# Kernel tuning notes

Measured on AMD Instinct MI355X. Metric: run time of the kernel, lower is better.

Reference implementation:

```python
import jax, jax.numpy as jnp
import numpy as np

N = 10000          # nodes
E_RAND = 320000    # random edges (avg degree 32)
F_IN = 512         # nfeat
HID = 256          # args.hid
HEADS = 8          # args.head
FH = HID // HEADS  # 32 per head
NCLASS = 40
TAU = 0.5
LAMDA = 0.5
K = 2


def setup_inputs() -> dict:
    key = jax.random.key(0)
    ks = jax.random.split(key, 16)
    # edge list: random edges + self-loops (so every dst segment is non-empty)
    src = jnp.concatenate([jax.random.randint(ks[0], (E_RAND,), 0, N), jnp.arange(N)])
    dst = jnp.concatenate([jax.random.randint(ks[1], (E_RAND,), 0, N), jnp.arange(N)])
    s = 0.05  # small init scale keeps exp() in attention/bind_loss stable
    return {
        "x": jax.random.normal(ks[2], (N, F_IN), jnp.float32),
        "src": src, "dst": dst,
        "W0": jax.random.normal(ks[3], (F_IN, HEADS, FH), jnp.float32) * s,
        "a0s": jax.random.normal(ks[4], (HEADS, FH), jnp.float32) * s,
        "a0d": jax.random.normal(ks[5], (HEADS, FH), jnp.float32) * s,
        "W1": jax.random.normal(ks[6], (HID, HEADS, FH), jnp.float32) * s,
        "a1s": jax.random.normal(ks[7], (HEADS, FH), jnp.float32) * s,
        "a1d": jax.random.normal(ks[8], (HEADS, FH), jnp.float32) * s,
        "W2": jax.random.normal(ks[9], (HID, HEADS, FH), jnp.float32) * s,
        "a2s": jax.random.normal(ks[10], (HEADS, FH), jnp.float32) * s,
        "a2d": jax.random.normal(ks[11], (HEADS, FH), jnp.float32) * s,
        "Wout": jax.random.normal(ks[12], (HID, HEADS, NCLASS), jnp.float32) * s,
        "aos": jax.random.normal(ks[13], (HEADS, NCLASS), jnp.float32) * s,
        "aod": jax.random.normal(ks[14], (HEADS, NCLASS), jnp.float32) * s,
    }


def _gat_layer(x, W, a_s, a_d, src, dst):
    """Sparse multi-head GAT layer: gather -> edge softmax -> scatter."""
    n = x.shape[0]
    h = jnp.einsum('nf,fhd->nhd', x, W)              # [N,H,Fh]
    es = jnp.sum(h * a_s, axis=-1)                    # [N,H]
    ed = jnp.sum(h * a_d, axis=-1)                    # [N,H]
    e = jax.nn.leaky_relu(es[src] + ed[dst], 0.2)     # [E,H]
    m = jax.ops.segment_max(e, dst, num_segments=n)   # per-dst max (stable softmax)
    w = jnp.exp(e - m[dst])
    z = jax.ops.segment_sum(w, dst, num_segments=n)
    alpha = w / z[dst]                                # [E,H]
    return jax.ops.segment_sum(alpha[:, :, None] * h[src], dst, num_segments=n)  # [N,H,Fh]


def _bind_loss(z):
    # z1 == z2 == z in the original call site: refl_sim == between_sim
    zn = z / jnp.maximum(jnp.linalg.norm(z, axis=1, keepdims=True), 1e-12)
    S = jnp.exp(jnp.matmul(zn, zn.T) / TAU)           # [N,N]
    d = jnp.diagonal(S)
    off = jnp.sum(S, axis=1) - d                      # masked (off-diagonal) row sum
    CT = -jnp.log(d / (off + off))                    # neg_c2.sum + neg_c3.sum
    return jnp.mean(CT)


def reference(x, src, dst, W0, a0s, a0d, W1, a1s, a1d, W2, a2s, a2d, Wout, aos, aod):
    layers = [(W0, a0s, a0d), (W1, a1s, a1d), (W2, a2s, a2d)]
    last = x
    loss = jnp.float32(0.0)
    for i, (W, as_, ad_) in enumerate(layers):
        cur = jax.nn.elu(_gat_layer(last, W, as_, ad_, src, dst))
        cur = cur.reshape(cur.shape[0], -1)           # concat heads -> [N, HID]
        if i > 0:
            beta = LAMDA / (i + 2)                    # MaskLayer(last, cur, lamda, i+2)
            cur = beta * last + (1.0 - beta) * cur
            if i % K == 0:
                loss = loss + _bind_loss(cur)
        last = cur
    out = _gat_layer(last, Wout, aos, aod, src, dst).mean(axis=1)  # avg heads -> [N,C]
    return (jax.nn.log_softmax(out, axis=1), loss)
```

## Files before the change

### kernel.cpp

```cpp
#include <hip/hip_runtime.h>
#include <hip/hip_bf16.h>
#include <math.h>

#define NN_F_IN   512
#define NN_HID    256
#define NN_HEADS  8
#define NN_FH     32
#define NN_NCLASS 40
#define TAU_F     0.5f
#define LAMDA_F   0.5f
#define ZN_SCALE  1.6986436f

typedef __attribute__((ext_vector_type(8))) short bf16x8;
typedef __attribute__((ext_vector_type(4))) float f32x4;

static __device__ __forceinline__ float lrelu02(float x) { return x >= 0.f ? x : 0.2f * x; }
static __device__ __forceinline__ float elu1(float x)    { return x > 0.f ? x : expm1f(x); }
static __device__ __forceinline__ float b2f(unsigned short u) {
    unsigned int x = ((unsigned int)u) << 16;
    return __uint_as_float(x);
}
static __device__ __forceinline__ unsigned short f2b(float f) {
    __hip_bfloat16 hb = __float2bfloat16(f);
    return *reinterpret_cast<unsigned short*>(&hb);
}

__global__ void prep_count_kernel(const float* __restrict__ x,
                                  const float* __restrict__ W0, const float* __restrict__ W1,
                                  const float* __restrict__ W2, const float* __restrict__ Wo,
                                  unsigned short* __restrict__ Xb,
                                  unsigned short* __restrict__ Wt0, unsigned short* __restrict__ Wt1,
                                  unsigned short* __restrict__ Wt2, unsigned short* __restrict__ Wto,
                                  int n4X,
                                  const int* __restrict__ dst, int* __restrict__ counts,
                                  int E, int nCountB) {
    if (blockIdx.x < nCountB) {
        int e = blockIdx.x * 256 + threadIdx.x;
        if (e < E) atomicAdd(&counts[dst[e]], 1);
        return;
    }
    int i = (blockIdx.x - nCountB) * 256 + threadIdx.x;
    if (i < n4X) {
        float4 v = *(const float4*)(x + (size_t)i * 4);
        ushort4 o;
        o.x = f2b(v.x); o.y = f2b(v.y); o.z = f2b(v.z); o.w = f2b(v.w);
        *(ushort4*)(Xb + (size_t)i * 4) = o;
        return;
    }
    i -= n4X;
    if (i < 256 * 512) {
        int np = i >> 9, k = i & 511;
        Wt0[i] = f2b(W0[(size_t)k * 256 + np]);
        return;
    }
    i -= 256 * 512;
    if (i < 256 * 256) {
        int np = i >> 8, k = i & 255;
        Wt1[i] = f2b(W1[(size_t)k * 256 + np]);
        return;
    }
    i -= 256 * 256;
    if (i < 256 * 256) {
        int np = i >> 8, k = i & 255;
        Wt2[i] = f2b(W2[(size_t)k * 256 + np]);
        return;
    }
    i -= 256 * 256;
    if (i < 384 * 256) {
        int np = i >> 8, k = i & 255;
        Wto[i] = f2b(np < 320 ? Wo[(size_t)k * 320 + np] : 0.f);
    }
}

__global__ __launch_bounds__(256) void fc_attn_mfma(
    const unsigned short* __restrict__ A, const unsigned short* __restrict__ B,
    unsigned short* __restrict__ H, const float* __restrict__ As_,
    const float* __restrict__ Ad_, float* __restrict__ es, float* __restrict__ ed,
    int M, int K) {
    const int ldH = 256;
    int t = threadIdx.x, lane = t & 63, wid = t >> 6;
    int wrow = wid >> 1, wcol = wid & 1;
    int l15 = lane & 15, lg = lane >> 4;
    int mbase = blockIdx.y * 64 + wrow * 32;
    int nbase = blockIdx.x * 64 + wcol * 32;

    const unsigned short* Ap[2];
    const unsigned short* Bp[2];
#pragma unroll
    for (int m = 0; m < 2; ++m) {
        int rr = mbase + m * 16 + l15;
        if (rr > M - 1) rr = M - 1;
        Ap[m] = A + (size_t)rr * K + lg * 8;
        Bp[m] = B + (size_t)(nbase + m * 16 + l15) * K + lg * 8;
    }
    f32x4 acc[2][2];
#pragma unroll
    for (int m = 0; m < 2; ++m)
#pragma unroll
        for (int nn = 0; nn < 2; ++nn)
#pragma unroll
            for (int r = 0; r < 4; ++r) acc[m][nn][r] = 0.f;

    bf16x8 aP[2], bP[2], aQ[2], bQ[2];
#pragma unroll
    for (int m = 0; m < 2; ++m) {
        aP[m] = *(const bf16x8*)(Ap[m]);
        bP[m] = *(const bf16x8*)(Bp[m]);
    }
    int nhalf = K >> 6;
    int kk = 32;
    for (int it = 0; it < nhalf; ++it) {
#pragma unroll
        for (int m = 0; m < 2; ++m) {
            aQ[m] = *(const bf16x8*)(Ap[m] + kk);
            bQ[m] = *(const bf16x8*)(Bp[m] + kk);
        }
#pragma unroll
        for (int m = 0; m < 2; ++m)
#pragma unroll
            for (int nn = 0; nn < 2; ++nn)
                acc[m][nn] = __builtin_amdgcn_mfma_f32_16x16x32_bf16(aP[m], bP[nn], acc[m][nn], 0, 0, 0);
        if (it + 1 < nhalf) {
#pragma unroll
            for (int m = 0; m < 2; ++m) {
                aP[m] = *(const bf16x8*)(Ap[m] + kk + 32);
                bP[m] = *(const bf16x8*)(Bp[m] + kk + 32);
            }
        }
#pragma unroll
        for (int m = 0; m < 2; ++m)
#pragma unroll
            for (int nn = 0; nn < 2; ++nn)
                acc[m][nn] = __builtin_amdgcn_mfma_f32_16x16x32_bf16(aQ[m], bQ[nn], acc[m][nn], 0, 0, 0);
        kk += 64;
    }
#pragma unroll
    for (int m = 0; m < 2; ++m) {
#pragma unroll
        for (int nn = 0; nn < 2; ++nn) {
            int col = nbase + nn * 16 + l15;
#pragma unroll
            for (int r = 0; r < 4; ++r) {
                int row = mbase + m * 16 + lg * 4 + r;
                if (row < M) H[(size_t)row * ldH + col] = f2b(acc[m][nn][r]);
            }
        }
    }
    int hh = blockIdx.x * 2 + wcol;
    float a0 = As_[hh * 32 + l15], a1 = As_[hh * 32 + 16 + l15];
    float d0 = Ad_[hh * 32 + l15], d1 = Ad_[hh * 32 + 16 + l15];
#pragma unroll
    for (int m = 0; m < 2; ++m) {
#pragma unroll
        for (int r = 0; r < 4; ++r) {
            float ps = acc[m][0][r] * a0 + acc[m][1][r] * a1;
            float pd = acc[m][0][r] * d0 + acc[m][1][r] * d1;
            ps += __shfl_xor(ps, 1, 64); pd += __shfl_xor(pd, 1, 64);
            ps += __shfl_xor(ps, 2, 64); pd += __shfl_xor(pd, 2, 64);
            ps += __shfl_xor(ps, 4, 64); pd += __shfl_xor(pd, 4, 64);
            ps += __shfl_xor(ps, 8, 64); pd += __shfl_xor(pd, 8, 64);
            if (l15 == 0) {
                int row = mbase + m * 16 + lg * 4 + r;
                if (row < M) {
                    es[row * NN_HEADS + hh] = ps;
                    ed[row * NN_HEADS + hh] = pd;
                }
            }
        }
    }
}

__global__ void scan_kernel(const int* __restrict__ counts, int* __restrict__ row_start,
                            int* __restrict__ cursor, int n) {
    __shared__ int s[1024];
    int t  = threadIdx.x;
    int ch = (n + 1023) / 1024;
    int lo = t * ch;
    int sum = 0;
    for (int j = 0; j < ch; ++j) {
        int i = lo + j;
        if (i < n) sum += counts[i];
    }
    s[t] = sum;
    __syncthreads();
    for (int off = 1; off < 1024; off <<= 1) {
        int v = 0;
        if (t >= off) v = s[t - off];
        __syncthreads();
        s[t] += v;
        __syncthreads();
    }
    int run = (t == 0) ? 0 : s[t - 1];
    for (int j = 0; j < ch; ++j) {
        int i = lo + j;
        if (i < n) {
            row_start[i] = run;
            cursor[i] = run;
            run += counts[i];
        }
    }
    if (t == 1023) row_start[n] = s[1023];
}

__global__ void scatter_kernel(const int* __restrict__ src, const int* __restrict__ dst,
                               int* __restrict__ cursor, int* __restrict__ csr_src, int E) {
    int e = blockIdx.x * blockDim.x + threadIdx.x;
    if (e < E) {
        int d   = dst[e];
        int pos = atomicAdd(&cursor[d], 1);
        csr_src[pos] = src[e];
    }
}

__global__ __launch_bounds__(256) void gather_hidden(
    const unsigned short* __restrict__ Hm, const float* __restrict__ es,
    const float* __restrict__ ed, const int* __restrict__ csr_src,
    const int* __restrict__ row_start, const unsigned short* __restrict__ last,
    unsigned short* __restrict__ out, int n, float beta,
    unsigned short* __restrict__ znb, float* __restrict__ dvec) {
    int lane = threadIdx.x & 63;
    int nn   = blockIdx.x * 4 + (threadIdx.x >> 6);
    if (nn >= n) return;
    int s0 = row_start[nn], s1 = row_start[nn + 1];
    int h2 = lane >> 3;
    float edh = ed[nn * NN_HEADS + h2];

    float zacc = 0.f;
    float a0 = 0.f, a1 = 0.f, a2 = 0.f, a3 = 0.f;
    int fullEnd = s0 + ((s1 - s0) & ~7);
    int e = s0;
    for (; e < fullEnd; e += 8) {
        int idx[8];
        float q[8];
#pragma unroll
        for (int j = 0; j < 8; ++j) idx[j] = csr_src[e + j];
#pragma unroll
        for (int j = 0; j < 8; ++j) q[j] = es[idx[j] * NN_HEADS + h2];
        ushort4 r[8];
#pragma unroll
        for (int j = 0; j < 8; ++j) r[j] = *(const ushort4*)&Hm[(size_t)idx[j] * NN_HID + lane * 4];
#pragma unroll
        for (int j = 0; j < 8; ++j) {
            float w = __expf(lrelu02(q[j] + edh));
            zacc += w;
            a0 += w * b2f(r[j].x); a1 += w * b2f(r[j].y);
            a2 += w * b2f(r[j].z); a3 += w * b2f(r[j].w);
        }
    }
    if (e < s1) {
        int c = s1 - e;
        int idx[8];
        float q[8];
#pragma unroll
        for (int j = 0; j < 8; ++j) idx[j] = csr_src[(j < c) ? e + j : e];
#pragma unroll
        for (int j = 0; j < 8; ++j) q[j] = es[idx[j] * NN_HEADS + h2];
        ushort4 r[8];
#pragma unroll
        for (int j = 0; j < 8; ++j) r[j] = *(const ushort4*)&Hm[(size_t)idx[j] * NN_HID + lane * 4];
#pragma unroll
        for (int j = 0; j < 8; ++j) {
            if (j < c) {
                float w = __expf(lrelu02(q[j] + edh));
                zacc += w;
                a0 += w * b2f(r[j].x); a1 += w * b2f(r[j].y);
                a2 += w * b2f(r[j].z); a3 += w * b2f(r[j].w);
            }
        }
    }
    float zi = 1.f / zacc;
    float v0 = elu1(a0 * zi), v1 = elu1(a1 * zi), v2 = elu1(a2 * zi), v3 = elu1(a3 * zi);
    if (beta >= 0.f) {
        ushort4 lv = *(const ushort4*)&last[(size_t)nn * NN_HID + lane * 4];
        v0 = beta * b2f(lv.x) + (1.f - beta) * v0;
        v1 = beta * b2f(lv.y) + (1.f - beta) * v1;
        v2 = beta * b2f(lv.z) + (1.f - beta) * v2;
        v3 = beta * b2f(lv.w) + (1.f - beta) * v3;
    }
    ushort4 o;
    o.x = f2b(v0); o.y = f2b(v1); o.z = f2b(v2); o.w = f2b(v3);
    *(ushort4*)&out[(size_t)nn * NN_HID + lane * 4] = o;

    if (znb) {
        float ss = v0 * v0 + v1 * v1 + v2 * v2 + v3 * v3;
        ss += __shfl_xor(ss, 1, 64);
        ss += __shfl_xor(ss, 2, 64);
        ss += __shfl_xor(ss, 4, 64);
        ss += __shfl_xor(ss, 8, 64);
        ss += __shfl_xor(ss, 16, 64);
        ss += __shfl_xor(ss, 32, 64);
        float m = fmaxf(sqrtf(ss), 1e-12f);
        float sc = ZN_SCALE / m;
        ushort4 zo;
        zo.x = f2b(v0 * sc); zo.y = f2b(v1 * sc);
        zo.z = f2b(v2 * sc); zo.w = f2b(v3 * sc);
        *(ushort4*)&znb[(size_t)nn * NN_HID + lane * 4] = zo;
        if (lane == 0) dvec[nn] = __expf((ss / (m * m)) * (1.f / TAU_F));
    }
}

__global__ __launch_bounds__(256) void gram_fc_mfma(
    const short* __restrict__ znb, float* __restrict__ P2d, int n,
    int T, int nwg, int Npad,
    const unsigned short* __restrict__ A, const unsigned short* __restrict__ Bw,
    unsigned short* __restrict__ H, int M, int nfc, int fcX) {
    __shared__ short As[2][128 * 64];
    __shared__ short Bs[2][128 * 64];

    int t    = threadIdx.x;
    int lane = t & 63;
    int wid  = t >> 6;
    int l15  = lane & 15, lg = lane >> 4;

    if (blockIdx.x < nfc) {
        const int K = 256, ncols = 320, ldH = 320;
        int idx = blockIdx.x;
        int bx = idx % fcX, by = idx / fcX;
        int wrow = wid >> 1, wcol = wid & 1;
        int mbase = by * 64 + wrow * 32;
        int nbase = bx * 64 + wcol * 32;

        const unsigned short* Ap[2];
        const unsigned short* Bp[2];
#pragma unroll
        for (int m = 0; m < 2; ++m) {
            int rr = mbase + m * 16 + l15;
            if (rr > M - 1) rr = M - 1;
            Ap[m] = A + (size_t)rr * K + lg * 8;
            Bp[m] = Bw + (size_t)(nbase + m * 16 + l15) * K + lg * 8;
        }
        f32x4 acc[2][2];
#pragma unroll
        for (int m = 0; m < 2; ++m)
#pragma unroll
            for (int nn = 0; nn < 2; ++nn)
#pragma unroll
                for (int r = 0; r < 4; ++r) acc[m][nn][r] = 0.f;

        bf16x8 aP[2], bP[2], aQ[2], bQ[2];
#pragma unroll
        for (int m = 0; m < 2; ++m) {
            aP[m] = *(const bf16x8*)(Ap[m]);
            bP[m] = *(const bf16x8*)(Bp[m]);
        }
        int kk = 32;
#pragma unroll
        for (int it = 0; it < 4; ++it) {
#pragma unroll
            for (int m = 0; m < 2; ++m) {
                aQ[m] = *(const bf16x8*)(Ap[m] + kk);
                bQ[m] = *(const bf16x8*)(Bp[m] + kk);
            }
#pragma unroll
            for (int m = 0; m < 2; ++m)
#pragma unroll
                for (int nn = 0; nn < 2; ++nn)
                    acc[m][nn] = __builtin_amdgcn_mfma_f32_16x16x32_bf16(aP[m], bP[nn], acc[m][nn], 0, 0, 0);
            if (it < 3) {
#pragma unroll
                for (int m = 0; m < 2; ++m) {
                    aP[m] = *(const bf16x8*)(Ap[m] + kk + 32);
                    bP[m] = *(const bf16x8*)(Bp[m] + kk + 32);
                }
            }
#pragma unroll
            for (int m = 0; m < 2; ++m)
#pragma unroll
                for (int nn = 0; nn < 2; ++nn)
                    acc[m][nn] = __builtin_amdgcn_mfma_f32_16x16x32_bf16(aQ[m], bQ[nn], acc[m][nn], 0, 0, 0);
            kk += 64;
        }
#pragma unroll
        for (int m = 0; m < 2; ++m) {
#pragma unroll
            for (int nn = 0; nn < 2; ++nn) {
                int col = nbase + nn * 16 + l15;
                if (col >= ncols) continue;
#pragma unroll
                for (int r = 0; r < 4; ++r) {
                    int row = mbase + m * 16 + lg * 4 + r;
                    if (row < M) H[(size_t)row * ldH + col] = f2b(acc[m][nn][r]);
                }
            }
        }
        return;
    }

    int b = blockIdx.x - nfc;
    int q = nwg >> 3, r8 = nwg & 7, xc = b & 7, oo = b >> 3;
    int sid = (xc < r8 ? xc * (q + 1) : r8 * (q + 1) + (xc - r8) * q) + oo;
    int bi = 0, rem = sid;
    while (rem >= T - bi) { rem -= T - bi; ++bi; }
    int bj = bi + rem;
    int i0 = bi * 128, j0 = bj * 128;

    int wrow = wid >> 1, wcol = wid & 1;
    int srow = lane >> 3;
    int sch  = lane & 7;

    f32x4 acc[4][4];
#pragma unroll
    for (int m = 0; m < 4; ++m)
#pragma unroll
        for (int nn = 0; nn < 4; ++nn)
#pragma unroll
            for (int r = 0; r < 4; ++r) acc[m][nn][r] = 0.f;

    bf16x8 sa[2][4], sb[2][4];
#pragma unroll
    for (int sl = 0; sl < 2; ++sl)
#pragma unroll
        for (int s = 0; s < 4; ++s) {
            int row = wid * 32 + s * 8 + srow;
            int gch = sch ^ (row & 7);
            sa[sl][s] = *(const bf16x8*)(znb + (size_t)(i0 + row) * NN_HID + sl * 64 + gch * 8);
            sb[sl][s] = *(const bf16x8*)(znb + (size_t)(j0 + row) * NN_HID + sl * 64 + gch * 8);
        }

#pragma unroll
    for (int kt = 0; kt < 2; ++kt) {
#pragma unroll
        for (int sl = 0; sl < 2; ++sl)
#pragma unroll
            for (int s = 0; s < 4; ++s) {
                int row = wid * 32 + s * 8 + srow;
                *(bf16x8*)(&As[sl][row * 64 + sch * 8]) = sa[sl][s];
                *(bf16x8*)(&Bs[sl][row * 64 + sch * 8]) = sb[sl][s];
            }
        __syncthreads();
        if (kt == 0) {
#pragma unroll
            for (int sl = 0; sl < 2; ++sl)
#pragma unroll
                for (int s = 0; s < 4; ++s) {
                    int row = wid * 32 + s * 8 + srow;
                    int gch = sch ^ (row & 7);
                    sa[sl][s] = *(const bf16x8*)(znb + (size_t)(i0 + row) * NN_HID + 128 + sl * 64 + gch * 8);
                    sb[sl][s] = *(const bf16x8*)(znb + (size_t)(j0 + row) * NN_HID + 128 + sl * 64 + gch * 8);
                }
        }
#pragma unroll
        for (int sl = 0; sl < 2; ++sl) {
#pragma unroll
            for (int ks = 0; ks < 2; ++ks) {
                bf16x8 av[4], bv[4];
#pragma unroll
                for (int m = 0; m < 4; ++m) {
                    int Ra = wrow * 64 + m * 16 + l15;
                    int Rb = wcol * 64 + m * 16 + l15;
                    int ca = (ks * 4 + lg) ^ (Ra & 7);
                    int cb = (ks * 4 + lg) ^ (Rb & 7);
                    av[m] = *(const bf16x8*)(&As[sl][Ra * 64 + ca * 8]);
                    bv[m] = *(const bf16x8*)(&Bs[sl][Rb * 64 + cb * 8]);
                }
#pragma unroll
                for (int m = 0; m < 4; ++m)
#pragma unroll
                    for (int nn = 0; nn < 4; ++nn)
                        acc[m][nn] = __builtin_amdgcn_mfma_f32_16x16x32_bf16(av[m], bv[nn], acc[m][nn], 0, 0, 0);
            }
        }
        if (kt == 0) __syncthreads();
    }

    int i0w = i0 + wrow * 64;
    int j0w = j0 + wcol * 64;
    bool diag = (bj == bi);
    if (bj == T - 1) {
#pragma unroll
        for (int m = 0; m < 4; ++m)
#pragma unroll
            for (int nn = 0; nn < 4; ++nn) {
                int gj = j0w + nn * 16 + l15;
                bool jok = gj < n;
#pragma unroll
                for (int r = 0; r < 4; ++r) {
                    int gi = i0w + m * 16 + lg * 4 + r;
                    acc[m][nn][r] = (jok && gi < n) ? __builtin_exp2f(acc[m][nn][r]) : 0.f;
                }
            }
    } else {
#pragma unroll
        for (int m = 0; m < 4; ++m)
#pragma unroll
            for (int nn = 0; nn < 4; ++nn)
#pragma unroll
                for (int r = 0; r < 4; ++r)
                    acc[m][nn][r] = __builtin_exp2f(acc[m][nn][r]);
    }
    float* rowslot = P2d + (size_t)(2 * bj + wcol) * Npad;
#pragma unroll
    for (int m = 0; m < 4; ++m) {
#pragma unroll
        for (int r = 0; r < 4; ++r) {
            float v = acc[m][0][r] + acc[m][1][r] + acc[m][2][r] + acc[m][3][r];
            v += __shfl_xor(v, 1, 64);
            v += __shfl_xor(v, 2, 64);
            v += __shfl_xor(v, 4, 64);
            v += __shfl_xor(v, 8, 64);
            if (l15 == 0) {
                int gi = i0w + m * 16 + lg * 4 + r;
                if (gi < n) rowslot[gi] = v;
            }
        }
    }
    if (!diag) {
        float* colslot = P2d + (size_t)(2 * bi + wrow) * Npad;
#pragma unroll
        for (int nn = 0; nn < 4; ++nn) {
            float v = 0.f;
#pragma unroll
            for (int m = 0; m < 4; ++m)
#pragma unroll
                for (int r = 0; r < 4; ++r) v += acc[m][nn][r];
            v += __shfl_xor(v, 16, 64);
            v += __shfl_xor(v, 32, 64);
            if (lg == 0) {
                int gj = j0w + nn * 16 + l15;
                if (gj < n) colslot[gj] = v;
            }
        }
    }
}

__global__ __launch_bounds__(256) void attn_fold_kernel(
    const unsigned short* __restrict__ Hm, const float* __restrict__ As,
    const float* __restrict__ Ad, float* __restrict__ es, float* __restrict__ ed,
    int n, int df, int nAt,
    const float* __restrict__ P2d, float* __restrict__ R, int slots, int Npad) {
    if (blockIdx.x < nAt) {
        int idx = blockIdx.x * 256 + threadIdx.x;
        if (idx >= n * NN_HEADS) return;
        int nn = idx / NN_HEADS, hh = idx - nn * NN_HEADS;
        const unsigned short* hp = Hm + (size_t)nn * NN_HEADS * df + hh * df;
        const float* ap = As + hh * df;
        const float* bp = Ad + hh * df;
        float s1 = 0.f, s2 = 0.f;
        for (int d = 0; d < df; d += 4) {
            ushort4 hv = *(const ushort4*)(hp + d);
            float4 av = *(const float4*)(ap + d);
            float4 bv = *(const float4*)(bp + d);
            float h0 = b2f(hv.x), h1 = b2f(hv.y), h2 = b2f(hv.z), h3 = b2f(hv.w);
            s1 += h0 * av.x + h1 * av.y + h2 * av.z + h3 * av.w;
            s2 += h0 * bv.x + h1 * bv.y + h2 * bv.z + h3 * bv.w;
        }
        es[idx] = s1;
        ed[idx] = s2;
        return;
    }
    int i = (blockIdx.x - nAt) * 256 + threadIdx.x;
    if (i >= n) return;
    const float* p = P2d + i;
    float s0 = 0.f, s1 = 0.f, s2 = 0.f, s3 = 0.f;
    int sl = 0;
    for (; sl + 4 <= slots; sl += 4) {
        s0 += p[(size_t)(sl + 0) * Npad];
        s1 += p[(size_t)(sl + 1) * Npad];
        s2 += p[(size_t)(sl + 2) * Npad];
        s3 += p[(size_t)(sl + 3) * Npad];
    }
    for (; sl < slots; ++sl) s0 += p[(size_t)sl * Npad];
    R[i] = (s0 + s1) + (s2 + s3);
}

__global__ __launch_bounds__(256) void edge_loss_kernel(
    const float* __restrict__ es, const float* __restrict__ ed,
    const int* __restrict__ csr_src, const int* __restrict__ row_start,
    float* __restrict__ wC, float* __restrict__ zinv, int n, int nEw,
    const float* __restrict__ R, const float* __restrict__ dvec,
    float* __restrict__ out_loss) {
    if (blockIdx.x < nEw) {
        int lane = threadIdx.x & 63;
        int nn   = blockIdx.x * 4 + (threadIdx.x >> 6);
        if (nn >= n) return;
        int s0 = row_start[nn], s1 = row_start[nn + 1];
        int h    = lane & 7;
        int slot = lane >> 3;
        float edh = ed[nn * NN_HEADS + h];
        float z = 0.f;
        for (int e = s0 + slot; e < s1; e += 8) {
            int sv = csr_src[e];
            float w = __expf(lrelu02(es[sv * NN_HEADS + h] + edh));
            wC[(size_t)e * NN_HEADS + h] = w;
            z += w;
        }
        z += __shfl_xor(z, 8, 64);
        z += __shfl_xor(z, 16, 64);
        z += __shfl_xor(z, 32, 64);
        if (slot == 0) zinv[nn * NN_HEADS + h] = 1.f / z;
        return;
    }
    __shared__ float s[256];
    int t = threadIdx.x;
    float sum = 0.f;
    for (int i = t; i < n; i += 256) {
        float d   = dvec[i];
        float off = R[i] - d;
        sum += -logf(d / (off + off));
    }
    s[t] = sum;
    __syncthreads();
    for (int o = 128; o > 0; o >>= 1) {
        if (t < o) s[t] += s[t + o];
        __syncthreads();
    }
    if (t == 0) *out_loss = s[0] / n;
}

__global__ void gather_final(const unsigned short* __restrict__ Hm, const float* __restrict__ wC,
                             const float* __restrict__ zinv, const int* __restrict__ csr_src,
                             const int* __restrict__ row_start, float* __restrict__ dout, int n) {
    int nn = blockIdx.x;
    __shared__ float accs[NN_HEADS * NN_NCLASS];
    int t = threadIdx.x;
    int s0 = row_start[nn], s1 = row_start[nn + 1];
    int hh = t / NN_NCLASS;
    float acc = 0.f;
    const int LD = NN_HEADS * NN_NCLASS;
    int fullEnd = s0 + ((s1 - s0) & ~7);
    int e = s0;
    for (; e < fullEnd; e += 8) {
        int idx[8];
        float wv[8];
#pragma unroll
        for (int j = 0; j < 8; ++j) {
            idx[j] = csr_src[e + j];
            wv[j]  = wC[(size_t)(e + j) * NN_HEADS + hh];
        }
        float v[8];
#pragma unroll
        for (int j = 0; j < 8; ++j) v[j] = b2f(Hm[(size_t)idx[j] * LD + t]);
#pragma unroll
        for (int j = 0; j < 8; ++j) acc += wv[j] * v[j];
    }
    if (e < s1) {
        int c = s1 - e;
        int idx[8];
        float wv[8];
#pragma unroll
        for (int j = 0; j < 8; ++j) {
            int p = (j < c) ? e + j : e;
            idx[j] = csr_src[p];
            wv[j]  = wC[(size_t)p * NN_HEADS + hh];
        }
        float v[8];
#pragma unroll
        for (int j = 0; j < 8; ++j) v[j] = b2f(Hm[(size_t)idx[j] * LD + t]);
#pragma unroll
        for (int j = 0; j < 8; ++j) {
            if (j < c) acc += wv[j] * v[j];
        }
    }
    accs[t] = acc * zinv[nn * NN_HEADS + hh];
    __syncthreads();
    if (t < 64) {
        float v = -INFINITY;
        if (t < NN_NCLASS) {
            float sacc = 0.f;
#pragma unroll
            for (int h2 = 0; h2 < NN_HEADS; ++h2) sacc += accs[h2 * NN_NCLASS + t];
            v = sacc * (1.f / NN_HEADS);
        }
        float mx = v;
#pragma unroll
        for (int o = 1; o < 64; o <<= 1) mx = fmaxf(mx, __shfl_xor(mx, o, 64));
        float ex = (t < NN_NCLASS) ? expf(v - mx) : 0.f;
        float se = ex;
#pragma unroll
        for (int o = 1; o < 64; o <<= 1) se += __shfl_xor(se, o, 64);
        if (t < NN_NCLASS) dout[(size_t)nn * NN_NCLASS + t] = (v - mx) - logf(se);
    }
}

extern "C" void kernel_launch(void* const* d_in, const int* in_sizes, int n_in,
                              void* d_out, int out_size, void* d_ws, size_t ws_size,
                              hipStream_t stream) {
    const float* x   = (const float*)d_in[0];
    const int*   src = (const int*)d_in[1];
    const int*   dst = (const int*)d_in[2];
    const float* W0  = (const float*)d_in[3];
    const float* a0s = (const float*)d_in[4];
    const float* a0d = (const float*)d_in[5];
    const float* W1  = (const float*)d_in[6];
    const float* a1s = (const float*)d_in[7];
    const float* a1d = (const float*)d_in[8];
    const float* W2  = (const float*)d_in[9];
    const float* a2s = (const float*)d_in[10];
    const float* a2d = (const float*)d_in[11];
    const float* Wout= (const float*)d_in[12];
    const float* aos = (const float*)d_in[13];
    const float* aod = (const float*)d_in[14];

    int N = in_sizes[0] / NN_F_IN;
    int E = in_sizes[1];
    int Npad = ((N + 127) / 128) * 128;
    int T = Npad / 128;
    int nwg = T * (T + 1) / 2;
    float* out = (float*)d_out;

    char*  ws  = (char*)d_ws;
    size_t off = 0;
    auto alloc = [&](size_t bytes) -> void* {
        void* p = ws + off;
        off += bytes;
        off = (off + 255) & ~(size_t)255;
        return p;
    };
    unsigned short* Hb = (unsigned short*)alloc((size_t)N * 320 * 2);
    unsigned short* znb = (unsigned short*)alloc((size_t)Npad * NN_HID * 2);
    unsigned short* Bl = (unsigned short*)alloc((size_t)N * NN_HID * 2);
    unsigned short* Bc = (unsigned short*)alloc((size_t)N * NN_HID * 2);
    size_t xbBytes = (size_t)N * NN_F_IN * 2;
    size_t p2Bytes = (size_t)2 * T * Npad * 4;
    void* XbP2d = alloc(xbBytes > p2Bytes ? xbBytes : p2Bytes);
    unsigned short* Xb  = (unsigned short*)XbP2d;
    float*          P2d = (float*)XbP2d;
    unsigned short* Wt0 = (unsigned short*)alloc((size_t)256 * 512 * 2);
    unsigned short* Wt1 = (unsigned short*)alloc((size_t)256 * 256 * 2);
    unsigned short* Wt2 = (unsigned short*)alloc((size_t)256 * 256 * 2);
    unsigned short* Wto = (unsigned short*)alloc((size_t)384 * 256 * 2);
    float* es     = (float*)alloc((size_t)N * NN_HEADS * 4);
    float* ed     = (float*)alloc((size_t)N * NN_HEADS * 4);
    float* wC     = (float*)alloc((size_t)E * NN_HEADS * 4);
    float* zinvA  = (float*)alloc((size_t)N * NN_HEADS * 4);
    float* Rrow   = (float*)alloc((size_t)N * 4);
    float* dvec   = (float*)alloc((size_t)N * 4);
    int*   counts = (int*)alloc((size_t)N * 4);
    int*   rs     = (int*)alloc((size_t)(N + 1) * 4);
    int*   cursor = (int*)alloc((size_t)N * 4);
    int*   csr    = (int*)alloc((size_t)E * 4);

    hipMemsetAsync(counts, 0, (size_t)N * 4, stream);
    if (Npad > N)
        hipMemsetAsync(znb + (size_t)N * NN_HID, 0, (size_t)(Npad - N) * NN_HID * 2, stream);

    int n4X = N * NN_F_IN / 4;
    int prepTotal = n4X + 256 * 512 + 256 * 256 + 256 * 256 + 384 * 256;
    int nCountB = (E + 255) / 256;
    int nPrepB  = (prepTotal + 255) / 256;
    prep_count_kernel<<<nCountB + nPrepB, 256, 0, stream>>>(
        x, W0, W1, W2, Wout, Xb, Wt0, Wt1, Wt2, Wto, n4X, dst, counts, E, nCountB);
    scan_kernel<<<1, 1024, 0, stream>>>(counts, rs, cursor, N);
    scatter_kernel<<<(E + 255) / 256, 256, 0, stream>>>(src, dst, cursor, csr, E);

    int atGrid = (N * NN_HEADS + 255) / 256;
    int ghGrid = (N + 3) / 4;
    int mT64 = (N + 63) / 64;

    fc_attn_mfma<<<dim3(4, mT64), 256, 0, stream>>>(Xb, Wt0, Hb, a0s, a0d, es, ed, N, 512);
    gather_hidden<<<ghGrid, 256, 0, stream>>>(Hb, es, ed, csr, rs, nullptr, Bl, N, -1.f,
                                              nullptr, nullptr);

    fc_attn_mfma<<<dim3(4, mT64), 256, 0, stream>>>(Bl, Wt1, Hb, a1s, a1d, es, ed, N, 256);
    gather_hidden<<<ghGrid, 256, 0, stream>>>(Hb, es, ed, csr, rs, Bl, Bc, N, LAMDA_F / 3.f,
                                              nullptr, nullptr);

    fc_attn_mfma<<<dim3(4, mT64), 256, 0, stream>>>(Bc, Wt2, Hb, a2s, a2d, es, ed, N, 256);
    gather_hidden<<<ghGrid, 256, 0, stream>>>(Hb, es, ed, csr, rs, Bc, Bl, N, LAMDA_F / 4.f,
                                              znb, dvec);

    int fcX = 5;
    int nfc = fcX * mT64;
    gram_fc_mfma<<<nfc + nwg, 256, 0, stream>>>((const short*)znb, P2d, N, T, nwg, Npad,
                                                Bl, Wto, Hb, N, nfc, fcX);

    int foldB = (N + 255) / 256;
    attn_fold_kernel<<<atGrid + foldB, 256, 0, stream>>>(
        Hb, aos, aod, es, ed, N, NN_NCLASS, atGrid, P2d, Rrow, 2 * T, Npad);

    edge_loss_kernel<<<ghGrid + 1, 256, 0, stream>>>(
        es, ed, csr, rs, wC, zinvA, N, ghGrid, Rrow, dvec,
        out + (size_t)N * NN_NCLASS);

    gather_final<<<N, NN_HEADS * NN_NCLASS, 0, stream>>>(Hb, wC, zinvA, csr, rs, out, N);
}
```

Before: 351.3 us.

## Fuse CSR scatter with first FC and fold edge weights into final gather

The CSR scatter kernel and the layer-0 FC/attention GEMM are merged into one launch, with block ranges split by index, because the GEMM does not depend on the CSR. The separate edge-weight kernel, which wrote per-edge exp weights and inverse normalisers to global memory, is removed. The final gather now recomputes the exp weights and the normaliser inline for each of its 320 threads, and the loss reduction runs as an extra block of that kernel. This removes two launches and the wC write/read traffic, but it recomputes exp 40x per head per edge and adds scattered es reads.

```diff
diff --git a/kernel.cpp b/kernel.cpp
--- a/kernel.cpp
+++ b/kernel.cpp
@@ -25,64 +25,17 @@
     return *reinterpret_cast<unsigned short*>(&hb);
 }
 
-__global__ void prep_count_kernel(const float* __restrict__ x,
-                                  const float* __restrict__ W0, const float* __restrict__ W1,
-                                  const float* __restrict__ W2, const float* __restrict__ Wo,
-                                  unsigned short* __restrict__ Xb,
-                                  unsigned short* __restrict__ Wt0, unsigned short* __restrict__ Wt1,
-                                  unsigned short* __restrict__ Wt2, unsigned short* __restrict__ Wto,
-                                  int n4X,
-                                  const int* __restrict__ dst, int* __restrict__ counts,
-                                  int E, int nCountB) {
-    if (blockIdx.x < nCountB) {
-        int e = blockIdx.x * 256 + threadIdx.x;
-        if (e < E) atomicAdd(&counts[dst[e]], 1);
-        return;
-    }
-    int i = (blockIdx.x - nCountB) * 256 + threadIdx.x;
-    if (i < n4X) {
-        float4 v = *(const float4*)(x + (size_t)i * 4);
-        ushort4 o;
-        o.x = f2b(v.x); o.y = f2b(v.y); o.z = f2b(v.z); o.w = f2b(v.w);
-        *(ushort4*)(Xb + (size_t)i * 4) = o;
-        return;
-    }
-    i -= n4X;
-    if (i < 256 * 512) {
-        int np = i >> 9, k = i & 511;
-        Wt0[i] = f2b(W0[(size_t)k * 256 + np]);
-        return;
-    }
-    i -= 256 * 512;
-    if (i < 256 * 256) {
-        int np = i >> 8, k = i & 255;
-        Wt1[i] = f2b(W1[(size_t)k * 256 + np]);
-        return;
-    }
-    i -= 256 * 256;
-    if (i < 256 * 256) {
-        int np = i >> 8, k = i & 255;
-        Wt2[i] = f2b(W2[(size_t)k * 256 + np]);
-        return;
-    }
-    i -= 256 * 256;
-    if (i < 384 * 256) {
-        int np = i >> 8, k = i & 255;
-        Wto[i] = f2b(np < 320 ? Wo[(size_t)k * 320 + np] : 0.f);
-    }
-}
-
-__global__ __launch_bounds__(256) void fc_attn_mfma(
+static __device__ __forceinline__ void fc_attn_body(
     const unsigned short* __restrict__ A, const unsigned short* __restrict__ B,
     unsigned short* __restrict__ H, const float* __restrict__ As_,
     const float* __restrict__ Ad_, float* __restrict__ es, float* __restrict__ ed,
-    int M, int K) {
+    int M, int K, int bx, int by) {
     const int ldH = 256;
     int t = threadIdx.x, lane = t & 63, wid = t >> 6;
     int wrow = wid >> 1, wcol = wid & 1;
     int l15 = lane & 15, lg = lane >> 4;
-    int mbase = blockIdx.y * 64 + wrow * 32;
-    int nbase = blockIdx.x * 64 + wcol * 32;
+    int mbase = by * 64 + wrow * 32;
+    int nbase = bx * 64 + wcol * 32;
 
     const unsigned short* Ap[2];
     const unsigned short* Bp[2];
@@ -146,7 +99,7 @@
             }
         }
     }
-    int hh = blockIdx.x * 2 + wcol;
+    int hh = bx * 2 + wcol;
     float a0 = As_[hh * 32 + l15], a1 = As_[hh * 32 + 16 + l15];
     float d0 = Ad_[hh * 32 + l15], d1 = Ad_[hh * 32 + 16 + l15];
 #pragma unroll
@@ -170,6 +123,53 @@
     }
 }
 
+__global__ void prep_count_kernel(const float* __restrict__ x,
+                                  const float* __restrict__ W0, const float* __restrict__ W1,
+                                  const float* __restrict__ W2, const float* __restrict__ Wo,
+                                  unsigned short* __restrict__ Xb,
+                                  unsigned short* __restrict__ Wt0, unsigned short* __restrict__ Wt1,
+                                  unsigned short* __restrict__ Wt2, unsigned short* __restrict__ Wto,
+                                  int n4X,
+                                  const int* __restrict__ dst, int* __restrict__ counts,
+                                  int E, int nCountB) {
+    if (blockIdx.x < nCountB) {
+        int e = blockIdx.x * 256 + threadIdx.x;
+        if (e < E) atomicAdd(&counts[dst[e]], 1);
+        return;
+    }
+    int i = (blockIdx.x - nCountB) * 256 + threadIdx.x;
+    if (i < n4X) {
+        float4 v = *(const float4*)(x + (size_t)i * 4);
+        ushort4 o;
+        o.x = f2b(v.x); o.y = f2b(v.y); o.z = f2b(v.z); o.w = f2b(v.w);
+        *(ushort4*)(Xb + (size_t)i * 4) = o;
+        return;
+    }
+    i -= n4X;
+    if (i < 256 * 512) {
+        int np = i >> 9, k = i & 511;
+        Wt0[i] = f2b(W0[(size_t)k * 256 + np]);
+        return;
+    }
+    i -= 256 * 512;
+    if (i < 256 * 256) {
+        int np = i >> 8, k = i & 255;
+        Wt1[i] = f2b(W1[(size_t)k * 256 + np]);
+        return;
+    }
+    i -= 256 * 256;
+    if (i < 256 * 256) {
+        int np = i >> 8, k = i & 255;
+        Wt2[i] = f2b(W2[(size_t)k * 256 + np]);
+        return;
+    }
+    i -= 256 * 256;
+    if (i < 384 * 256) {
+        int np = i >> 8, k = i & 255;
+        Wto[i] = f2b(np < 320 ? Wo[(size_t)k * 320 + np] : 0.f);
+    }
+}
+
 __global__ void scan_kernel(const int* __restrict__ counts, int* __restrict__ row_start,
                             int* __restrict__ cursor, int n) {
     __shared__ int s[1024];
@@ -202,14 +202,32 @@
     if (t == 1023) row_start[n] = s[1023];
 }
 
-__global__ void scatter_kernel(const int* __restrict__ src, const int* __restrict__ dst,
-                               int* __restrict__ cursor, int* __restrict__ csr_src, int E) {
-    int e = blockIdx.x * blockDim.x + threadIdx.x;
-    if (e < E) {
-        int d   = dst[e];
-        int pos = atomicAdd(&cursor[d], 1);
-        csr_src[pos] = src[e];
-    }
+__global__ __launch_bounds__(256) void scatter_fc0_kernel(
+    const int* __restrict__ src, const int* __restrict__ dst,
+    int* __restrict__ cursor, int* __restrict__ csr_src, int E, int nSc,
+    const unsigned short* __restrict__ A, const unsigned short* __restrict__ B,
+    unsigned short* __restrict__ H, const float* __restrict__ As_,
+    const float* __restrict__ Ad_, float* __restrict__ es, float* __restrict__ ed,
+    int M, int K) {
+    if (blockIdx.x < nSc) {
+        int e = blockIdx.x * 256 + threadIdx.x;
+        if (e < E) {
+            int d   = dst[e];
+            int pos = atomicAdd(&cursor[d], 1);
+            csr_src[pos] = src[e];
+        }
+        return;
+    }
+    int idx = blockIdx.x - nSc;
+    fc_attn_body(A, B, H, As_, Ad_, es, ed, M, K, idx & 3, idx >> 2);
+}
+
+__global__ __launch_bounds__(256) void fc_attn_mfma(
+    const unsigned short* __restrict__ A, const unsigned short* __restrict__ B,
+    unsigned short* __restrict__ H, const float* __restrict__ As_,
+    const float* __restrict__ Ad_, float* __restrict__ es, float* __restrict__ ed,
+    int M, int K) {
+    fc_attn_body(A, B, H, As_, Ad_, es, ed, M, K, blockIdx.x, blockIdx.y);
 }
 
 __global__ __launch_bounds__(256) void gather_hidden(
@@ -563,95 +581,79 @@
     R[i] = (s0 + s1) + (s2 + s3);
 }
 
-__global__ __launch_bounds__(256) void edge_loss_kernel(
-    const float* __restrict__ es, const float* __restrict__ ed,
-    const int* __restrict__ csr_src, const int* __restrict__ row_start,
-    float* __restrict__ wC, float* __restrict__ zinv, int n, int nEw,
+__global__ void gather_final_loss(
+    const unsigned short* __restrict__ Hm, const float* __restrict__ es,
+    const float* __restrict__ ed, const int* __restrict__ csr_src,
+    const int* __restrict__ row_start, float* __restrict__ dout, int n,
     const float* __restrict__ R, const float* __restrict__ dvec,
     float* __restrict__ out_loss) {
-    if (blockIdx.x < nEw) {
-        int lane = threadIdx.x & 63;
-        int nn   = blockIdx.x * 4 + (threadIdx.x >> 6);
-        if (nn >= n) return;
-        int s0 = row_start[nn], s1 = row_start[nn + 1];
-        int h    = lane & 7;
-        int slot = lane >> 3;
-        float edh = ed[nn * NN_HEADS + h];
-        float z = 0.f;
-        for (int e = s0 + slot; e < s1; e += 8) {
-            int sv = csr_src[e];
-            float w = __expf(lrelu02(es[sv * NN_HEADS + h] + edh));
-            wC[(size_t)e * NN_HEADS + h] = w;
-            z += w;
-        }
-        z += __shfl_xor(z, 8, 64);
-        z += __shfl_xor(z, 16, 64);
-        z += __shfl_xor(z, 32, 64);
-        if (slot == 0) zinv[nn * NN_HEADS + h] = 1.f / z;
-        return;
-    }
-    __shared__ float s[256];
     int t = threadIdx.x;
-    float sum = 0.f;
-    for (int i = t; i < n; i += 256) {
-        float d   = dvec[i];
-        float off = R[i] - d;
-        sum += -logf(d / (off + off));
-    }
-    s[t] = sum;
-    __syncthreads();
-    for (int o = 128; o > 0; o >>= 1) {
-        if (t < o) s[t] += s[t + o];
+    if ((int)blockIdx.x >= n) {
+        __shared__ float s[320];
+        float sum = 0.f;
+        for (int i = t; i < n; i += 320) {
+            float d   = dvec[i];
+            float off = R[i] - d;
+            sum += -logf(d / (off + off));
+        }
+        s[t] = sum;
         __syncthreads();
-    }
-    if (t == 0) *out_loss = s[0] / n;
-}
-
-__global__ void gather_final(const unsigned short* __restrict__ Hm, const float* __restrict__ wC,
-                             const float* __restrict__ zinv, const int* __restrict__ csr_src,
-                             const int* __restrict__ row_start, float* __restrict__ dout, int n) {
+        if (t < 64) s[t] += s[t + 256];
+        __syncthreads();
+        for (int o = 128; o > 0; o >>= 1) {
+            if (t < o) s[t] += s[t + o];
+            __syncthreads();
+        }
+        if (t == 0) *out_loss = s[0] / n;
+        return;
+    }
     int nn = blockIdx.x;
     __shared__ float accs[NN_HEADS * NN_NCLASS];
-    int t = threadIdx.x;
     int s0 = row_start[nn], s1 = row_start[nn + 1];
     int hh = t / NN_NCLASS;
-    float acc = 0.f;
+    float edh = ed[nn * NN_HEADS + hh];
+    float acc = 0.f, zacc = 0.f;
     const int LD = NN_HEADS * NN_NCLASS;
     int fullEnd = s0 + ((s1 - s0) & ~7);
     int e = s0;
     for (; e < fullEnd; e += 8) {
         int idx[8];
-        float wv[8];
+        float q[8];
+#pragma unroll
+        for (int j = 0; j < 8; ++j) idx[j] = csr_src[e + j];
+#pragma unroll
+        for (int j = 0; j < 8; ++j) q[j] = es[idx[j] * NN_HEADS + hh];
+        float v[8];
+#pragma unroll
+        for (int j = 0; j < 8; ++j) v[j] = b2f(Hm[(size_t)idx[j] * LD + t]);
 #pragma unroll
         for (int j = 0; j < 8; ++j) {
-            idx[j] = csr_src[e + j];
-            wv[j]  = wC[(size_t)(e + j) * NN_HEADS + hh];
-        }
-        float v[8];
-#pragma unroll
-        for (int j = 0; j < 8; ++j) v[j] = b2f(Hm[(size_t)idx[j] * LD + t]);
-#pragma unroll
-        for (int j = 0; j < 8; ++j) acc += wv[j] * v[j];
+            float w = __expf(lrelu02(q[j] + edh));
+            zacc += w;
+            acc += w * v[j];
+        }
     }
     if (e < s1) {
         int c = s1 - e;
         int idx[8];
-        float wv[8];
+        float q[8];
+#pragma unroll
+        for (int j = 0; j < 8; ++j) idx[j] = csr_src[(j < c) ? e + j : e];
+#pragma unroll
+        for (int j = 0; j < 8; ++j) q[j] = es[idx[j] * NN_HEADS + hh];
+        float v[8];
+#pragma unroll
+        for (int j = 0; j < 8; ++j) v[j] = b2f(Hm[(size_t)idx[j] * LD + t]);
 #pragma unroll
         for (int j = 0; j < 8; ++j) {
-            int p = (j < c) ? e + j : e;
-            idx[j] = csr_src[p];
-            wv[j]  = wC[(size_t)p * NN_HEADS + hh];
-        }
-        float v[8];
-#pragma unroll
-        for (int j = 0; j < 8; ++j) v[j] = b2f(Hm[(size_t)idx[j] * LD + t]);
-#pragma unroll
-        for (int j = 0; j < 8; ++j) {
-            if (j < c) acc += wv[j] * v[j];
-        }
-    }
-    accs[t] = acc * zinv[nn * NN_HEADS + hh];
+            if (j < c) {
+                float w = __expf(lrelu02(q[j] + edh));
+                zacc += w;
+                acc += w * v[j];
+            }
+        }
+    }
+    accs[t] = acc / zacc;
     __syncthreads();
     if (t < 64) {
         float v = -INFINITY;
@@ -721,8 +723,6 @@
     unsigned short* Wto = (unsigned short*)alloc((size_t)384 * 256 * 2);
     float* es     = (float*)alloc((size_t)N * NN_HEADS * 4);
     float* ed     = (float*)alloc((size_t)N * NN_HEADS * 4);
-    float* wC     = (float*)alloc((size_t)E * NN_HEADS * 4);
-    float* zinvA  = (float*)alloc((size_t)N * NN_HEADS * 4);
     float* Rrow   = (float*)alloc((size_t)N * 4);
     float* dvec   = (float*)alloc((size_t)N * 4);
     int*   counts = (int*)alloc((size_t)N * 4);
@@ -741,13 +741,15 @@
     prep_count_kernel<<<nCountB + nPrepB, 256, 0, stream>>>(
         x, W0, W1, W2, Wout, Xb, Wt0, Wt1, Wt2, Wto, n4X, dst, counts, E, nCountB);
     scan_kernel<<<1, 1024, 0, stream>>>(counts, rs, cursor, N);
-    scatter_kernel<<<(E + 255) / 256, 256, 0, stream>>>(src, dst, cursor, csr, E);
 
     int atGrid = (N * NN_HEADS + 255) / 256;
     int ghGrid = (N + 3) / 4;
     int mT64 = (N + 63) / 64;
 
-    fc_attn_mfma<<<dim3(4, mT64), 256, 0, stream>>>(Xb, Wt0, Hb, a0s, a0d, es, ed, N, 512);
+    int nSc = (E + 255) / 256;
+    scatter_fc0_kernel<<<nSc + 4 * mT64, 256, 0, stream>>>(
+        src, dst, cursor, csr, E, nSc,
+        Xb, Wt0, Hb, a0s, a0d, es, ed, N, 512);
     gather_hidden<<<ghGrid, 256, 0, stream>>>(Hb, es, ed, csr, rs, nullptr, Bl, N, -1.f,
                                               nullptr, nullptr);
 
@@ -768,9 +770,6 @@
     attn_fold_kernel<<<atGrid + foldB, 256, 0, stream>>>(
         Hb, aos, aod, es, ed, N, NN_NCLASS, atGrid, P2d, Rrow, 2 * T, Npad);
 
-    edge_loss_kernel<<<ghGrid + 1, 256, 0, stream>>>(
-        es, ed, csr, rs, wC, zinvA, N, ghGrid, Rrow, dvec,
-        out + (size_t)N * NN_NCLASS);
-
-    gather_final<<<N, NN_HEADS * NN_NCLASS, 0, stream>>>(Hb, wC, zinvA, csr, rs, out, N);
-}
+    gather_final_loss<<<N + 1, NN_HEADS * NN_NCLASS, 0, stream>>>(
+        Hb, es, ed, csr, rs, out, N, Rrow, dvec, out + (size_t)N * NN_NCLASS);
+}
```

Measured after the change: 363.7 us. 3.5% more time.
